# Performance work log

Hardware: AMD Instinct MI355X
Metric: run time of the kernel (lower is better)

## Reference

```python
import jax, jax.numpy as jnp
import numpy as np

B, C, M, T = 2, 512, 16, 128
H = 8
D = C // H  # 64, divisible by 4 for 2D RoPE
G = C // 4  # GroupNorm groups = 128
S = M * T


def group_norm(x, scale, bias, groups=G, eps=1e-5):
    b, c, m, t = x.shape
    xg = x.reshape(b, groups, c // groups, m, t)
    mu = xg.mean(axis=(2, 3, 4), keepdims=True)
    var = xg.var(axis=(2, 3, 4), keepdims=True)
    xn = ((xg - mu) * jax.lax.rsqrt(var + eps)).reshape(b, c, m, t)
    return xn * scale[None, :, None, None] + bias[None, :, None, None]


def dwsep_conv(x, dw, pw):
    # depthwise 3x3 (groups=C) then pointwise 1x1
    y = jax.lax.conv_general_dilated(
        x, dw, window_strides=(1, 1), padding='SAME',
        dimension_numbers=('NCHW', 'HWIO', 'NCHW'), feature_group_count=x.shape[1])
    return jnp.einsum('bcmt,cd->bdmt', y, pw)


def rope2d(x):
    # x: [B,H,M,T,D]; first D/2 dims rotated by freq index m, last D/2 by time index t
    d = x.shape[-1]
    dh = d // 2
    q = dh // 2
    inv = 1.0 / (10000.0 ** (jnp.arange(q, dtype=jnp.float32) / q))

    def rot(v, ang):
        h = v.shape[-1] // 2
        v1, v2 = v[..., :h], v[..., h:]
        c, s = jnp.cos(ang), jnp.sin(ang)
        return jnp.concatenate([v1 * c - v2 * s, v1 * s + v2 * c], axis=-1)

    ang_f = jnp.arange(x.shape[2], dtype=jnp.float32)[:, None] * inv  # [M,q]
    ang_t = jnp.arange(x.shape[3], dtype=jnp.float32)[:, None] * inv  # [T,q]
    xf = rot(x[..., :dh], ang_f[:, None, :])  # broadcast over T
    xt = rot(x[..., dh:], ang_t)
    return jnp.concatenate([xf, xt], axis=-1)


def setup_inputs() -> dict:
    key = jax.random.key(0)
    ks = jax.random.split(key, 14)
    s = 0.02
    return {
        'x': jax.random.normal(ks[0], (B, C, M, T), jnp.float32),
        'lengths': jax.random.randint(ks[1], (B,), T // 2, T + 1),
        'gn_scale': jnp.ones((C,), jnp.float32),
        'gn_bias': jnp.zeros((C,), jnp.float32),
        'dw_q': jax.random.normal(ks[2], (3, 3, 1, C), jnp.float32) * s,
        'dw_k': jax.random.normal(ks[3], (3, 3, 1, C), jnp.float32) * s,
        'dw_v': jax.random.normal(ks[4], (3, 3, 1, C), jnp.float32) * s,
        'pw_q': jax.random.normal(ks[5], (C, C), jnp.float32) * s,
        'pw_k': jax.random.normal(ks[6], (C, C), jnp.float32) * s,
        'pw_v': jax.random.normal(ks[7], (C, C), jnp.float32) * s,
        'attn_w': jax.random.normal(ks[8], (C, C), jnp.float32) * s,
        'attn_b': jnp.zeros((C,), jnp.float32),
        'out_w': jax.random.normal(ks[9], (C, C), jnp.float32) * s,
        'out_b': jnp.zeros((C,), jnp.float32),
    }


def reference(x, lengths, gn_scale, gn_bias, dw_q, dw_k, dw_v, pw_q, pw_k, pw_v,
              attn_w, attn_b, out_w, out_b):
    residual = x
    xn = group_norm(x, gn_scale, gn_bias)

    def to_heads(y):  # [B,C,M,T] -> [B,H,M,T,D]
        return y.reshape(B, H, D, M, T).transpose(0, 1, 3, 4, 2)

    q = rope2d(to_heads(dwsep_conv(xn, dw_q, pw_q)))
    k = rope2d(to_heads(dwsep_conv(xn, dw_k, pw_k)))
    v = to_heads(dwsep_conv(xn, dw_v, pw_v))

    q = q.reshape(B, H, S, D)
    k = k.reshape(B, H, S, D)
    v = v.reshape(B, H, S, D)

    scores = jnp.einsum('bhsd,bhkd->bhsk', q, k) / np.sqrt(D).astype(np.float32)
    valid_t = jnp.arange(T)[None, :] < lengths[:, None]        # [B,T]
    valid = jnp.tile(valid_t, (1, M))                          # [B,S], token idx = m*T + t
    scores = jnp.where(valid[:, None, None, :], scores, jnp.float32(-1e9))
    attn = jax.nn.softmax(scores, axis=-1)
    o = jnp.einsum('bhsk,bhkd->bhsd', attn, v)                 # [B,H,S,D]

    o = o.transpose(0, 2, 1, 3).reshape(B, S, C)
    o = o @ attn_w + attn_b                                    # block output proj
    o = o.reshape(B, M, T, C).transpose(0, 3, 1, 2)            # [B,C,M,T]
    out = jnp.einsum('bcmt,cd->bdmt', o, out_w) + out_b[None, :, None, None]
    return residual + out
```

## Files before the change

kernel.cpp:

```cpp
#include <hip/hip_runtime.h>
#include <math.h>

#define CCH 512
#define SSQ 2048
#define MTOT 4096

typedef __bf16 bf16;
typedef __bf16 bf16x8 __attribute__((ext_vector_type(8)));
typedef __bf16 bf16x4 __attribute__((ext_vector_type(4)));
typedef float  f32x4  __attribute__((ext_vector_type(4)));

#define AS1 __attribute__((address_space(1)))
#define AS3 __attribute__((address_space(3)))
__device__ __forceinline__ void glds16(const void* g, void* l) {
    __builtin_amdgcn_global_load_lds((const AS1 void*)g, (AS3 void*)l, 16, 0, 0);
}

__global__ __launch_bounds__(256) void gnw_kernel(const float* __restrict__ x,
        float* __restrict__ mu, float* __restrict__ rstd,
        const float* __restrict__ w0, const float* __restrict__ w1,
        const float* __restrict__ w2, const float* __restrict__ w3,
        const float* __restrict__ w4, bf16* __restrict__ wT,
        const float* __restrict__ attnb, const float* __restrict__ outb,
        float* __restrict__ bcv) {
    __shared__ float smem[64*65];
    int tid = threadIdx.x;
    if (blockIdx.x < 256) {
        float* s_sum = smem;
        float* s_sq  = smem + 256;
        int bg = blockIdx.x;
        long base = (long)bg * 8192;
        float sum = 0.f, sq = 0.f;
#pragma unroll
        for (int r = 0; r < 32; ++r) {
            float v = x[base + r*256 + tid];
            sum += v; sq += v*v;
        }
        s_sum[tid] = sum; s_sq[tid] = sq;
        __syncthreads();
        for (int off = 128; off > 0; off >>= 1) {
            if (tid < off) { s_sum[tid] += s_sum[tid+off]; s_sq[tid] += s_sq[tid+off]; }
            __syncthreads();
        }
        if (tid == 0) {
            float m = s_sum[0] * (1.f/8192.f);
            float v = s_sq[0]  * (1.f/8192.f) - m*m;
            mu[bg] = m;
            rstd[bg] = rsqrtf(v + 1e-5f);
        }
    } else if (blockIdx.x < 576) {
        int bid = blockIdx.x - 256;
        int z = bid >> 6, r2 = bid & 63;
        int k0 = (r2 >> 3)*64, n0 = (r2 & 7)*64;
        const float* srcs[5] = {w0, w1, w2, w3, w4};
        const float* W = srcs[z];
        bf16* D = wT + (long)z * (CCH*CCH);
        float (*t)[65] = (float(*)[65])smem;
        int cI = tid & 63, r4 = tid >> 6;
#pragma unroll
        for (int p = 0; p < 16; ++p) {
            int kr = p*4 + r4;
            t[kr][cI] = W[(long)(k0+kr)*CCH + n0 + cI];
        }
        __syncthreads();
#pragma unroll
        for (int p = 0; p < 16; ++p) {
            int nr = p*4 + r4;
            D[(long)(n0+nr)*CCH + k0 + cI] = (bf16)t[cI][nr];
        }
    } else if (blockIdx.x < 578) {
        int n = (blockIdx.x - 576)*256 + tid;
        float a = outb[n];
#pragma unroll 16
        for (int j = 0; j < 512; ++j)
            a = fmaf(attnb[j], w4[(long)j*CCH + n], a);
        bcv[n] = a;
    } else {
        bf16* wAc = wT + (long)5*CCH*CCH;
        int base = (blockIdx.x - 578)*4096 + tid;
#pragma unroll
        for (int p = 0; p < 16; ++p)
            wAc[base + p*256] = (bf16)w3[base + p*256];
    }
}

__global__ void tn_kernel(const float* __restrict__ x, const float* __restrict__ mu,
                          const float* __restrict__ rstd, const float* __restrict__ gsc,
                          const float* __restrict__ gbs, bf16* __restrict__ xnT) {
    __shared__ float t[64][65];
    int s0 = blockIdx.x*64, c0 = blockIdx.y*64, b = blockIdx.z;
    int tid = threadIdx.x;
    int cI = tid & 63, r4 = tid >> 6;
#pragma unroll
    for (int p = 0; p < 16; ++p) {
        int cr = p*4 + r4;
        t[cr][cI] = x[((long)(b*CCH + c0 + cr))*SSQ + s0 + cI];
    }
    __syncthreads();
#pragma unroll
    for (int p = 0; p < 16; ++p) {
        int sr = p*4 + r4;
        int c = c0 + cI;
        int g = b*128 + (c >> 2);
        float v = (t[cI][sr] - mu[g]) * rstd[g] * gsc[c] + gbs[c];
        xnT[((long)(b*SSQ + s0 + sr))*CCH + c] = (bf16)v;
    }
}

__global__ __launch_bounds__(256) void dw3_kernel(const bf16* __restrict__ xnT,
        const float* __restrict__ dwq, const float* __restrict__ dwk,
        const float* __restrict__ dwv,
        bf16* __restrict__ yq, bf16* __restrict__ yk, bf16* __restrict__ yv) {
    int tid = threadIdx.x;
    int cc = (tid & 63) * 8;
    int s  = blockIdx.x*4 + (tid >> 6);
    int sl = s & (SSQ-1);
    int b  = s >> 11;
    int m = sl >> 7, t = sl & 127;
    float aq[8] = {}, ak[8] = {}, av[8] = {};
#pragma unroll
    for (int di = 0; di < 3; ++di) {
        int m2 = m + di - 1;
        if ((unsigned)m2 >= 16u) continue;
#pragma unroll
        for (int dj = 0; dj < 3; ++dj) {
            int t2 = t + dj - 1;
            if ((unsigned)t2 >= 128u) continue;
            bf16x8 xv = *(const bf16x8*)(xnT + ((long)(b*SSQ + m2*128 + t2))*CCH + cc);
            int wi = (di*3 + dj)*CCH + cc;
#pragma unroll
            for (int i = 0; i < 8; ++i) {
                float xf = (float)xv[i];
                aq[i] += xf * dwq[wi+i];
                ak[i] += xf * dwk[wi+i];
                av[i] += xf * dwv[wi+i];
            }
        }
    }
    bf16x8 oq, ok, ov;
#pragma unroll
    for (int i = 0; i < 8; ++i) { oq[i] = (bf16)aq[i]; ok[i] = (bf16)ak[i]; ov[i] = (bf16)av[i]; }
    long o = (long)s*CCH + cc;
    *(bf16x8*)(yq + o) = oq;
    *(bf16x8*)(yk + o) = ok;
    *(bf16x8*)(yv + o) = ov;
}

template<int NFR>
__device__ __forceinline__ void gemm_core128(const bf16* __restrict__ A,
        const bf16* __restrict__ Wt, int m0, int n0,
        bf16* As, bf16* Bs, f32x4 (&acc)[4][NFR]) {
    int tid = threadIdx.x, lane = tid & 63, wid = tid >> 6;
    int sw = wid & 1, nw = wid >> 1;
    int col = lane & 15, quad = lane >> 4;
    const char* gA[4]; char* ldsA[4];
#pragma unroll
    for (int p = 0; p < 4; ++p) {
        int ci = tid + p*256;
        int row = ci >> 3;
        int c = (ci & 7) ^ (row & 7);
        gA[p] = (const char*)A + ((long)(m0+row)*CCH + c*8)*2;
        ldsA[p] = (char*)As + ci*16;
    }
    const char* gB[NFR]; char* ldsB[NFR];
#pragma unroll
    for (int p = 0; p < NFR; ++p) {
        int ci = tid + p*256;
        int row = ci >> 3;
        int c = (ci & 7) ^ (row & 7);
        gB[p] = (const char*)Wt + ((long)(n0+row)*CCH + c*8)*2;
        ldsB[p] = (char*)Bs + ci*16;
    }
    int rowA = sw*64 + col;
    int rowB = nw*(NFR*16) + col;
    for (int k0 = 0; k0 < CCH; k0 += 64) {
        __syncthreads();
#pragma unroll
        for (int p = 0; p < 4; ++p)   glds16(gA[p] + k0*2, ldsA[p]);
#pragma unroll
        for (int p = 0; p < NFR; ++p) glds16(gB[p] + k0*2, ldsB[p]);
        __syncthreads();
        bf16x8 af[4][2], bfr[NFR][2];
#pragma unroll
        for (int mt = 0; mt < 4; ++mt) {
            int r = rowA + mt*16;
#pragma unroll
            for (int ks = 0; ks < 2; ++ks) {
                int c = (ks*4 + quad) ^ (r & 7);
                af[mt][ks] = *(const bf16x8*)((char*)As + r*128 + c*16);
            }
        }
#pragma unroll
        for (int nt = 0; nt < NFR; ++nt) {
            int r = rowB + nt*16;
#pragma unroll
            for (int ks = 0; ks < 2; ++ks) {
                int c = (ks*4 + quad) ^ (r & 7);
                bfr[nt][ks] = *(const bf16x8*)((char*)Bs + r*128 + c*16);
            }
        }
#pragma unroll
        for (int ks = 0; ks < 2; ++ks)
#pragma unroll
            for (int mt = 0; mt < 4; ++mt)
#pragma unroll
                for (int nt = 0; nt < NFR; ++nt)
                    acc[mt][nt] = __builtin_amdgcn_mfma_f32_16x16x32_bf16(
                        af[mt][ks], bfr[nt][ks], acc[mt][nt], 0,0,0);
    }
}

__global__ __launch_bounds__(256) void gemm_qkv(const bf16* __restrict__ Abase,
        bf16* __restrict__ wT, bf16* __restrict__ qout,
        bf16* __restrict__ kout, bf16* __restrict__ vout) {
    __shared__ bf16 As[128*64];
    __shared__ bf16 Bs[64*64];
    int z = blockIdx.z;
    if (z == 3 && blockIdx.x >= 4) return;
    int m0 = blockIdx.x*128, n0 = blockIdx.y*64;
    const bf16* Aop = (z < 3) ? Abase + (long)z*MTOT*CCH : wT + (long)4*CCH*CCH;
    const bf16* Wop = (z < 3) ? wT + (long)z*CCH*CCH   : wT + (long)5*CCH*CCH;
    f32x4 acc[4][2] = {};
    gemm_core128<2>(Aop, Wop, m0, n0, As, Bs, acc);
    int tid = threadIdx.x, lane = tid & 63, wid = tid >> 6;
    int sw = wid & 1, nw = wid >> 1;
    int col = lane & 15, quad = lane >> 4;
    int nb = n0 + nw*32, mb = m0 + sw*64;
    if (z == 3) {
        bf16* wCt = wT + (long)6*CCH*CCH;
#pragma unroll
        for (int nt = 0; nt < 2; ++nt) {
            int n = nb + nt*16 + col;
#pragma unroll
            for (int mt = 0; mt < 4; ++mt)
#pragma unroll
                for (int r = 0; r < 4; ++r)
                    wCt[(long)(mb + mt*16 + quad*4 + r)*CCH + n] = (bf16)acc[mt][nt][r];
        }
    } else if (z < 2) {
        bf16* outp = z ? kout : qout;
        const float sc = z ? 1.0f : 0.125f;
        float invf = __expf(-(float)col * 0.5756462732485114f);
        bool tHalf = (nb & 32) != 0;
#pragma unroll
        for (int mt = 0; mt < 4; ++mt)
#pragma unroll
            for (int r = 0; r < 4; ++r) {
                int row = mb + mt*16 + quad*4 + r;
                int sl = row & (SSQ-1);
                float pos = tHalf ? (float)(sl & 127) : (float)(sl >> 7);
                float ang = pos * invf;
                float sn, cs;
                __sincosf(ang, &sn, &cs);
                float x1 = acc[mt][0][r], x2 = acc[mt][1][r];
                outp[(long)row*CCH + nb + col]      = (bf16)((x1*cs - x2*sn)*sc);
                outp[(long)row*CCH + nb + 16 + col] = (bf16)((x1*sn + x2*cs)*sc);
            }
    } else {
#pragma unroll
        for (int mt = 0; mt < 4; ++mt)
#pragma unroll
            for (int nt = 0; nt < 2; ++nt) {
                int n = nb + nt*16 + col;
                int row0 = mb + mt*16 + quad*4;
                int bq = row0 >> 11, sl0 = row0 & (SSQ-1);
                int sub16 = (sl0 >> 4) & 1;
                long slp = (long)(sl0 & ~31) + quad*8 + sub16*4;
                bf16x4 pk;
#pragma unroll
                for (int r = 0; r < 4; ++r) pk[r] = (bf16)acc[mt][nt][r];
                *(bf16x4*)(vout + ((long)(bq*CCH + n))*SSQ + slp) = pk;
            }
    }
}

__global__ __launch_bounds__(256) void gemm_out(const bf16* __restrict__ A,
        const bf16* __restrict__ Wt, const float* __restrict__ bias,
        const float* __restrict__ resid, float* __restrict__ outp) {
    __shared__ bf16 As[128*64];
    __shared__ bf16 Bs[64*64];
    int m0 = blockIdx.x*128, n0 = blockIdx.y*64;
    f32x4 acc[4][2] = {};
    gemm_core128<2>(A, Wt, m0, n0, As, Bs, acc);
    int tid = threadIdx.x, lane = tid & 63, wid = tid >> 6;
    int sw = wid & 1, nw = wid >> 1;
    int col = lane & 15, quad = lane >> 4;
    int nb = n0 + nw*32, mb = m0 + sw*64;
#pragma unroll
    for (int mt = 0; mt < 4; ++mt)
#pragma unroll
        for (int nt = 0; nt < 2; ++nt) {
            int n = nb + nt*16 + col;
            float bv = bias[n];
            int row0 = mb + mt*16 + quad*4;
            int b = row0 >> 11, sl0 = row0 & (SSQ-1);
            long off = ((long)(b*CCH + n))*SSQ + sl0;
            float4 rr = *(const float4*)(resid + off);
            float4 o4;
            o4.x = acc[mt][nt][0] + bv + rr.x;
            o4.y = acc[mt][nt][1] + bv + rr.y;
            o4.z = acc[mt][nt][2] + bv + rr.z;
            o4.w = acc[mt][nt][3] + bv + rr.w;
            *(float4*)(outp + off) = o4;
        }
}

__global__ __launch_bounds__(256, 2) void attn_kernel(
        const bf16* __restrict__ qb, const bf16* __restrict__ kb,
        const bf16* __restrict__ vb, const int* __restrict__ lengths,
        bf16* __restrict__ o) {
    __shared__ char KVs[2][32768];
    __shared__ float Lsm[4][4][16];
    int bid = blockIdx.x;
    int bh = bid & 15, qtb = bid >> 4;
    int b = bh >> 3, h = bh & 7;
    int tid = threadIdx.x, wid = tid >> 6, lane = tid & 63;
    int col = lane & 15, quad = lane >> 4;
    int q0 = qtb*64;
    int lenb = lengths[b];
    int thr = lenb - wid*32 - quad*4;

    const char* gK[4]; const char* gV[4];
#pragma unroll
    for (int j = 0; j < 4; ++j) {
        int s = j*64 + lane;
        int rl = s >> 3;
        int cin = s & 7;
        int csrc = cin ^ (rl & 7);
        gK[j] = (const char*)kb + ((long)(b*SSQ + wid*32 + rl))*1024 + h*128 + csrc*16;
        gV[j] = (const char*)vb + ((long)(b*CCH + h*64 + j*16 + col))*4096 + (wid*4 + quad)*16;
    }
    char* ldsK = (char*)KVs + wid*4096 + lane*16;
    char* ldsV = (char*)KVs + 16384 + wid*4096 + lane*16;

    const bf16* qp = qb + (long)(b*SSQ)*CCH + h*64;
    bf16x8 qf[4][2];
#pragma unroll
    for (int qt = 0; qt < 4; ++qt)
#pragma unroll
        for (int dc = 0; dc < 2; ++dc)
            qf[qt][dc] = *(const bf16x8*)(qp + (long)(q0 + qt*16 + col)*CCH + dc*32 + quad*8);

    f32x4 of[4][4] = {};
    float ls[4] = {};
    int cswz7 = col & 7;
    int kc0 = (quad ^ cswz7)*16;
    int kc1 = ((4 + quad) ^ cswz7)*16;

#pragma unroll
    for (int j = 0; j < 4; ++j) glds16(gK[j], ldsK + j*1024);
#pragma unroll
    for (int j = 0; j < 4; ++j) glds16(gV[j], ldsV + j*1024);
#pragma unroll
    for (int j = 0; j < 4; ++j) glds16(gK[j] + 131072L, ldsK + 32768 + j*1024);
#pragma unroll
    for (int j = 0; j < 4; ++j) glds16(gV[j] + 256L, ldsV + 32768 + j*1024);

    for (int t = 0; t < 16; ++t) {
        if (t == 15) { asm volatile("s_waitcnt vmcnt(0)" ::: "memory"); }
        else         { asm volatile("s_waitcnt vmcnt(8)" ::: "memory"); }
        __builtin_amdgcn_sched_barrier(0);
        const char* K = KVs[t & 1] + wid*4096;
        const char* V = KVs[t & 1] + 16384 + wid*4096;
        bf16x8 kf[2][2], vf[4];
#pragma unroll
        for (int sub = 0; sub < 2; ++sub) {
            kf[sub][0] = *(const bf16x8*)(K + sub*2048 + col*128 + kc0);
            kf[sub][1] = *(const bf16x8*)(K + sub*2048 + col*128 + kc1);
        }
#pragma unroll
        for (int dt = 0; dt < 4; ++dt)
            vf[dt] = *(const bf16x8*)(V + dt*1024 + lane*16);
        asm volatile("s_waitcnt lgkmcnt(0)" ::: "memory");
        __builtin_amdgcn_sched_barrier(0);
        if (t < 14) {
            int bsel = (t & 1)*32768;
#pragma unroll
            for (int j = 0; j < 4; ++j) glds16(gK[j] + (long)(t+2)*131072, ldsK + bsel + j*1024);
#pragma unroll
            for (int j = 0; j < 4; ++j) glds16(gV[j] + (long)(t+2)*256,    ldsV + bsel + j*1024);
        }
        __builtin_amdgcn_sched_barrier(0);
        f32x4 sc[2][4];
#pragma unroll
        for (int sub = 0; sub < 2; ++sub) {
            f32x4 m;
#pragma unroll
            for (int r = 0; r < 4; ++r) m[r] = (sub*16 + r < thr) ? 0.f : -10000.f;
#pragma unroll
            for (int qt = 0; qt < 4; ++qt) sc[sub][qt] = m;
        }
        __builtin_amdgcn_s_setprio(1);
#pragma unroll
        for (int sub = 0; sub < 2; ++sub)
#pragma unroll
            for (int qt = 0; qt < 4; ++qt) {
                sc[sub][qt] = __builtin_amdgcn_mfma_f32_16x16x32_bf16(kf[sub][0], qf[qt][0], sc[sub][qt], 0,0,0);
                sc[sub][qt] = __builtin_amdgcn_mfma_f32_16x16x32_bf16(kf[sub][1], qf[qt][1], sc[sub][qt], 0,0,0);
            }
        __builtin_amdgcn_s_setprio(0);
        bf16x8 pf[4];
#pragma unroll
        for (int qt = 0; qt < 4; ++qt) {
            float s = 0.f;
#pragma unroll
            for (int r = 0; r < 4; ++r) {
                float e0 = __expf(sc[0][qt][r]);
                float e1 = __expf(sc[1][qt][r]);
                pf[qt][r]     = (bf16)e0;
                pf[qt][4 + r] = (bf16)e1;
                s += e0 + e1;
            }
            ls[qt] += s;
        }
        __builtin_amdgcn_s_setprio(1);
#pragma unroll
        for (int dt = 0; dt < 4; ++dt)
#pragma unroll
            for (int qt = 0; qt < 4; ++qt)
                of[qt][dt] = __builtin_amdgcn_mfma_f32_16x16x32_bf16(pf[qt], vf[dt], of[qt][dt], 0,0,0);
        __builtin_amdgcn_s_setprio(0);
    }

#pragma unroll
    for (int qt = 0; qt < 4; ++qt) {
        ls[qt] += __shfl_xor(ls[qt], 16);
        ls[qt] += __shfl_xor(ls[qt], 32);
    }
    __syncthreads();
    float* Om = (float*)KVs;
#pragma unroll
    for (int qt = 0; qt < 4; ++qt)
#pragma unroll
        for (int dt = 0; dt < 4; ++dt)
#pragma unroll
            for (int r = 0; r < 4; ++r)
                Om[(wid*64 + qt*16 + quad*4 + r)*64 + dt*16 + col] = of[qt][dt][r];
    if (quad == 0)
#pragma unroll
        for (int qt = 0; qt < 4; ++qt) Lsm[wid][qt][col] = ls[qt];
    __syncthreads();
    bf16* ob = o + (long)(b*SSQ + q0)*CCH + h*64;
#pragma unroll
    for (int i = 0; i < 16; ++i) {
        int rr = wid*16 + i;
        float v = Om[rr*64 + lane] + Om[(64 + rr)*64 + lane]
                + Om[(128 + rr)*64 + lane] + Om[(192 + rr)*64 + lane];
        float l = Lsm[0][wid][i] + Lsm[1][wid][i] + Lsm[2][wid][i] + Lsm[3][wid][i];
        ob[(long)rr*CCH + lane] = (bf16)(v / l);
    }
}

extern "C" void kernel_launch(void* const* d_in, const int* in_sizes, int n_in,
                              void* d_out, int out_size, void* d_ws, size_t ws_size,
                              hipStream_t stream) {
    const float* x        = (const float*)d_in[0];
    const int*   lengths  = (const int*)  d_in[1];
    const float* gn_scale = (const float*)d_in[2];
    const float* gn_bias  = (const float*)d_in[3];
    const float* dw_q     = (const float*)d_in[4];
    const float* dw_k     = (const float*)d_in[5];
    const float* dw_v     = (const float*)d_in[6];
    const float* pw_q     = (const float*)d_in[7];
    const float* pw_k     = (const float*)d_in[8];
    const float* pw_v     = (const float*)d_in[9];
    const float* attn_w   = (const float*)d_in[10];
    const float* attn_b   = (const float*)d_in[11];
    const float* out_w    = (const float*)d_in[12];
    const float* out_b    = (const float*)d_in[13];
    float* out = (float*)d_out;

    char* w = (char*)d_ws;
    float* mu   = (float*)w;
    float* rstd = (float*)(w + 1024);
    float* bcv  = (float*)(w + 2048);
    bf16* wT    = (bf16*)(w + 4096);
    bf16* wCt = wT + (long)6*CCH*CCH;
    bf16* xnT  = (bf16*)(w + 0x00400000);
    bf16* yT   = (bf16*)(w + 0x00800000);
    bf16* qbf  = (bf16*)(w + 0x01400000);
    bf16* kbf  = (bf16*)(w + 0x01800000);
    bf16* vbf  = (bf16*)(w + 0x01C00000);
    bf16* obf  = (bf16*)(w + 0x02000000);

    gnw_kernel<<<642, 256, 0, stream>>>(x, mu, rstd, pw_q, pw_k, pw_v, attn_w, out_w,
                                        wT, attn_b, out_b, bcv);
    tn_kernel<<<dim3(32,8,2), 256, 0, stream>>>(x, mu, rstd, gn_scale, gn_bias, xnT);
    dw3_kernel<<<MTOT/4, 256, 0, stream>>>(xnT, dw_q, dw_k, dw_v,
                                           yT, yT + (long)MTOT*CCH, yT + (long)2*MTOT*CCH);

    gemm_qkv<<<dim3(MTOT/128, CCH/64, 4), 256, 0, stream>>>(yT, wT, qbf, kbf, vbf);

    attn_kernel<<<512, 256, 0, stream>>>(qbf, kbf, vbf, lengths, obf);

    gemm_out<<<dim3(MTOT/128, CCH/64), 256, 0, stream>>>(obf, wCt, bcv, x, out);
}
```

Before: 162.1 us.

## Fuse groupnorm-transpose with depthwise conv and double-buffer GEMM LDS loads

Merges the normalize/transpose kernel and the depthwise 3x3 conv into one kernel that normalizes three frequency bands of x into a swizzled LDS tile and convolves from LDS. This removes the bf16 xnT intermediate round trip and one launch, at the cost of recomputing neighbouring bands per block and fewer blocks. The shared GEMM core now double-buffers its LDS tiles so the next K-slice load overlaps MFMA work, doubling LDS use per block.

```diff
diff --git a/kernel.cpp b/kernel.cpp
--- a/kernel.cpp
+++ b/kernel.cpp
@@ -84,66 +84,74 @@
     }
 }
 
-__global__ void tn_kernel(const float* __restrict__ x, const float* __restrict__ mu,
-                          const float* __restrict__ rstd, const float* __restrict__ gsc,
-                          const float* __restrict__ gbs, bf16* __restrict__ xnT) {
-    __shared__ float t[64][65];
-    int s0 = blockIdx.x*64, c0 = blockIdx.y*64, b = blockIdx.z;
-    int tid = threadIdx.x;
-    int cI = tid & 63, r4 = tid >> 6;
-#pragma unroll
-    for (int p = 0; p < 16; ++p) {
-        int cr = p*4 + r4;
-        t[cr][cI] = x[((long)(b*CCH + c0 + cr))*SSQ + s0 + cI];
-    }
-    __syncthreads();
-#pragma unroll
-    for (int p = 0; p < 16; ++p) {
-        int sr = p*4 + r4;
-        int c = c0 + cI;
-        int g = b*128 + (c >> 2);
-        float v = (t[cI][sr] - mu[g]) * rstd[g] * gsc[c] + gbs[c];
-        xnT[((long)(b*SSQ + s0 + sr))*CCH + c] = (bf16)v;
-    }
-}
-
-__global__ __launch_bounds__(256) void dw3_kernel(const bf16* __restrict__ xnT,
+__global__ __launch_bounds__(256) void tndw_kernel(const float* __restrict__ x,
+        const float* __restrict__ mu, const float* __restrict__ rstd,
+        const float* __restrict__ gsc, const float* __restrict__ gbs,
         const float* __restrict__ dwq, const float* __restrict__ dwk,
         const float* __restrict__ dwv,
         bf16* __restrict__ yq, bf16* __restrict__ yk, bf16* __restrict__ yv) {
+    __shared__ bf16 xn[3][128][72];
+    int m = blockIdx.x, c0 = blockIdx.y*64, b = blockIdx.z;
     int tid = threadIdx.x;
-    int cc = (tid & 63) * 8;
-    int s  = blockIdx.x*4 + (tid >> 6);
-    int sl = s & (SSQ-1);
-    int b  = s >> 11;
-    int m = sl >> 7, t = sl & 127;
-    float aq[8] = {}, ak[8] = {}, av[8] = {};
-#pragma unroll
-    for (int di = 0; di < 3; ++di) {
-        int m2 = m + di - 1;
-        if ((unsigned)m2 >= 16u) continue;
-#pragma unroll
-        for (int dj = 0; dj < 3; ++dj) {
-            int t2 = t + dj - 1;
-            if ((unsigned)t2 >= 128u) continue;
-            bf16x8 xv = *(const bf16x8*)(xnT + ((long)(b*SSQ + m2*128 + t2))*CCH + cc);
-            int wi = (di*3 + dj)*CCH + cc;
-#pragma unroll
-            for (int i = 0; i < 8; ++i) {
-                float xf = (float)xv[i];
-                aq[i] += xf * dwq[wi+i];
-                ak[i] += xf * dwk[wi+i];
-                av[i] += xf * dwv[wi+i];
-            }
-        }
-    }
-    bf16x8 oq, ok, ov;
-#pragma unroll
-    for (int i = 0; i < 8; ++i) { oq[i] = (bf16)aq[i]; ok[i] = (bf16)ak[i]; ov[i] = (bf16)av[i]; }
-    long o = (long)s*CCH + cc;
-    *(bf16x8*)(yq + o) = oq;
-    *(bf16x8*)(yk + o) = ok;
-    *(bf16x8*)(yv + o) = ov;
+#pragma unroll
+    for (int band = 0; band < 3; ++band) {
+        int mm = m + band - 1;
+        if ((unsigned)mm >= 16u) continue;
+        const float* xb = x + ((long)(b*CCH + c0))*SSQ + mm*128;
+#pragma unroll
+        for (int p = 0; p < 8; ++p) {
+            int idx = p*256 + tid;
+            int c_l = idx >> 5;
+            int t4 = (idx & 31) * 4;
+            float4 v4 = *(const float4*)(xb + (long)c_l*SSQ + t4);
+            int c = c0 + c_l;
+            int g = b*128 + (c >> 2);
+            float mu_ = mu[g], rs = rstd[g], sc_ = gsc[c], bs_ = gbs[c];
+            int chunk = c_l >> 3, coff = c_l & 7;
+            const float* vv = &v4.x;
+#pragma unroll
+            for (int j = 0; j < 4; ++j) {
+                int t = t4 + j;
+                int cc2 = (chunk + ((t >> 2) & 7)) & 7;
+                xn[band][t][cc2*8 + coff] = (bf16)((vv[j] - mu_) * rs * sc_ + bs_);
+            }
+        }
+    }
+    __syncthreads();
+    int c8 = tid & 7, tq = tid >> 3;
+    long obase = ((long)(b*SSQ + m*128))*CCH + c0 + c8*8;
+#pragma unroll
+    for (int ti = 0; ti < 4; ++ti) {
+        int t = tq + ti*32;
+        float aq[8] = {}, ak[8] = {}, av[8] = {};
+#pragma unroll
+        for (int band = 0; band < 3; ++band) {
+            int mm = m + band - 1;
+            if ((unsigned)mm >= 16u) continue;
+#pragma unroll
+            for (int dj = 0; dj < 3; ++dj) {
+                int t2 = t + dj - 1;
+                if ((unsigned)t2 >= 128u) continue;
+                int cc2 = (c8 + ((t2 >> 2) & 7)) & 7;
+                bf16x8 xv = *(const bf16x8*)(&xn[band][t2][cc2*8]);
+                int wi = (band*3 + dj)*CCH + c0 + c8*8;
+#pragma unroll
+                for (int i = 0; i < 8; ++i) {
+                    float xf = (float)xv[i];
+                    aq[i] += xf * dwq[wi+i];
+                    ak[i] += xf * dwk[wi+i];
+                    av[i] += xf * dwv[wi+i];
+                }
+            }
+        }
+        bf16x8 oq, ok, ov;
+#pragma unroll
+        for (int i = 0; i < 8; ++i) { oq[i] = (bf16)aq[i]; ok[i] = (bf16)ak[i]; ov[i] = (bf16)av[i]; }
+        long o = obase + (long)t*CCH;
+        *(bf16x8*)(yq + o) = oq;
+        *(bf16x8*)(yk + o) = ok;
+        *(bf16x8*)(yv + o) = ov;
+    }
 }
 
 template<int NFR>
@@ -173,13 +181,22 @@
     }
     int rowA = sw*64 + col;
     int rowB = nw*(NFR*16) + col;
+#pragma unroll
+    for (int p = 0; p < 4; ++p)   glds16(gA[p], ldsA[p]);
+#pragma unroll
+    for (int p = 0; p < NFR; ++p) glds16(gB[p], ldsB[p]);
+    __syncthreads();
+    int buf = 0;
     for (int k0 = 0; k0 < CCH; k0 += 64) {
-        __syncthreads();
-#pragma unroll
-        for (int p = 0; p < 4; ++p)   glds16(gA[p] + k0*2, ldsA[p]);
-#pragma unroll
-        for (int p = 0; p < NFR; ++p) glds16(gB[p] + k0*2, ldsB[p]);
-        __syncthreads();
+        if (k0 + 64 < CCH) {
+            int nb = buf ^ 1;
+#pragma unroll
+            for (int p = 0; p < 4; ++p)   glds16(gA[p] + (k0+64)*2, ldsA[p] + nb*16384);
+#pragma unroll
+            for (int p = 0; p < NFR; ++p) glds16(gB[p] + (k0+64)*2, ldsB[p] + nb*(NFR*4096));
+        }
+        const char* Ab = (const char*)As + buf*16384;
+        const char* Bb = (const char*)Bs + buf*(NFR*4096);
         bf16x8 af[4][2], bfr[NFR][2];
 #pragma unroll
         for (int mt = 0; mt < 4; ++mt) {
@@ -187,7 +204,7 @@
 #pragma unroll
             for (int ks = 0; ks < 2; ++ks) {
                 int c = (ks*4 + quad) ^ (r & 7);
-                af[mt][ks] = *(const bf16x8*)((char*)As + r*128 + c*16);
+                af[mt][ks] = *(const bf16x8*)(Ab + r*128 + c*16);
             }
         }
 #pragma unroll
@@ -196,7 +213,7 @@
 #pragma unroll
             for (int ks = 0; ks < 2; ++ks) {
                 int c = (ks*4 + quad) ^ (r & 7);
-                bfr[nt][ks] = *(const bf16x8*)((char*)Bs + r*128 + c*16);
+                bfr[nt][ks] = *(const bf16x8*)(Bb + r*128 + c*16);
             }
         }
 #pragma unroll
@@ -207,14 +224,16 @@
                 for (int nt = 0; nt < NFR; ++nt)
                     acc[mt][nt] = __builtin_amdgcn_mfma_f32_16x16x32_bf16(
                         af[mt][ks], bfr[nt][ks], acc[mt][nt], 0,0,0);
+        __syncthreads();
+        buf ^= 1;
     }
 }
 
 __global__ __launch_bounds__(256) void gemm_qkv(const bf16* __restrict__ Abase,
         bf16* __restrict__ wT, bf16* __restrict__ qout,
         bf16* __restrict__ kout, bf16* __restrict__ vout) {
-    __shared__ bf16 As[128*64];
-    __shared__ bf16 Bs[64*64];
+    __shared__ bf16 As[2*128*64];
+    __shared__ bf16 Bs[2*2*32*64];
     int z = blockIdx.z;
     if (z == 3 && blockIdx.x >= 4) return;
     int m0 = blockIdx.x*128, n0 = blockIdx.y*64;
@@ -277,8 +296,8 @@
 __global__ __launch_bounds__(256) void gemm_out(const bf16* __restrict__ A,
         const bf16* __restrict__ Wt, const float* __restrict__ bias,
         const float* __restrict__ resid, float* __restrict__ outp) {
-    __shared__ bf16 As[128*64];
-    __shared__ bf16 Bs[64*64];
+    __shared__ bf16 As[2*128*64];
+    __shared__ bf16 Bs[2*2*32*64];
     int m0 = blockIdx.x*128, n0 = blockIdx.y*64;
     f32x4 acc[4][2] = {};
     gemm_core128<2>(A, Wt, m0, n0, As, Bs, acc);
@@ -476,7 +495,6 @@
     float* bcv  = (float*)(w + 2048);
     bf16* wT    = (bf16*)(w + 4096);
     bf16* wCt = wT + (long)6*CCH*CCH;
-    bf16* xnT  = (bf16*)(w + 0x00400000);
     bf16* yT   = (bf16*)(w + 0x00800000);
     bf16* qbf  = (bf16*)(w + 0x01400000);
     bf16* kbf  = (bf16*)(w + 0x01800000);
@@ -485,9 +503,9 @@
 
     gnw_kernel<<<642, 256, 0, stream>>>(x, mu, rstd, pw_q, pw_k, pw_v, attn_w, out_w,
                                         wT, attn_b, out_b, bcv);
-    tn_kernel<<<dim3(32,8,2), 256, 0, stream>>>(x, mu, rstd, gn_scale, gn_bias, xnT);
-    dw3_kernel<<<MTOT/4, 256, 0, stream>>>(xnT, dw_q, dw_k, dw_v,
-                                           yT, yT + (long)MTOT*CCH, yT + (long)2*MTOT*CCH);
+    tndw_kernel<<<dim3(16, 8, 2), 256, 0, stream>>>(x, mu, rstd, gn_scale, gn_bias,
+                                                    dw_q, dw_k, dw_v,
+                                                    yT, yT + (long)MTOT*CCH, yT + (long)2*MTOT*CCH);
 
     gemm_qkv<<<dim3(MTOT/128, CCH/64, 4), 256, 0, stream>>>(yT, wT, qbf, kbf, vbf);
 
```

Measured after the change: 171.0 us. 5.5% more time.
